# Kernel optimization log

Measured on AMD Instinct MI355X. Metric: run time of the kernel, lower is better.

The kernel has to match this reference:

```python
import jax, jax.numpy as jnp
import numpy as np

N_INIT = jnp.array([17.047, 14.099, 3.625], dtype=jnp.float32)
CA_INIT = jnp.array([16.967, 12.784, 4.338], dtype=jnp.float32)
C_INIT = jnp.array([15.685, 12.755, 5.133], dtype=jnp.float32)


def _unit(x):
    return x / (jnp.linalg.norm(x, axis=-1, keepdims=True) + 1e-8)


def _place_dihedral(a, b, c, bond_angle, bond_length, torsion):
    # a,b,c: [B,3]; bond_angle/bond_length/torsion: [B]
    ab = b - a
    bc = _unit(c - b)
    cr = jnp.cross(ab, bc)
    crn = jnp.linalg.norm(cr, axis=-1, keepdims=True)
    n_main = _unit(cr)
    # collinear fallback (per-element; almost never triggers for real angles)
    perp = jnp.zeros_like(bc).at[..., 0].set(1.0)
    ct = jnp.cross(bc, perp)
    ctn = jnp.linalg.norm(ct, axis=-1, keepdims=True)
    perp2 = jnp.where(ctn < 1e-6, jnp.zeros_like(bc).at[..., 1].set(1.0), perp)
    n_fb = _unit(jnp.cross(bc, perp2))
    n = jnp.where(crn < 1e-6, n_fb, n_main)
    nbc = jnp.cross(n, bc)
    m = jnp.stack([bc, nbc, n], axis=-1)  # [B,3,3]
    d_local = jnp.stack([
        -bond_length * jnp.cos(bond_angle),
        bond_length * jnp.cos(torsion) * jnp.sin(bond_angle),
        bond_length * jnp.sin(torsion) * jnp.sin(bond_angle),
    ], axis=-1)  # [B,3]
    d = jnp.einsum('bij,bj->bi', m, d_local)
    return d + c


def _nerf_build(phi, psi, omega, bond_lengths, bond_angles):
    B, L = phi.shape
    init = jnp.broadcast_to(jnp.stack([N_INIT, CA_INIT, C_INIT]), (B, 3, 3))
    # per-step params, leading axis = residue index i in [0, L-2]
    xs = (
        psi[:, :L - 1].T,                 # psi_i
        omega[:, :L - 1].T,               # omega_i
        phi[:, 1:].T,                     # phi_{i+1}
        bond_lengths[:, :L - 1, 2].T,     # C-N length
        bond_lengths[:, :L - 1, 0].T,     # N-CA length
        bond_lengths[:, :L - 1, 1].T,     # CA-C length
        bond_angles[:, :L - 1, 1].T,      # CA-C-N angle
        bond_angles[:, :L - 1, 2].T,      # C-N-CA angle
        bond_angles[:, :L - 1, 0].T,      # N-CA-C angle
    )

    def step(prev, x):
        psi_i, omega_i, phi_i, len_cn, len_nca, len_cac, ang_cacn, ang_cnca, ang_ncac = x
        a, b, c = prev[:, 0], prev[:, 1], prev[:, 2]
        n = _place_dihedral(a, b, c, ang_cacn, len_cn, psi_i)
        ca = _place_dihedral(b, c, n, ang_cnca, len_nca, omega_i)
        cc = _place_dihedral(c, n, ca, ang_ncac, len_cac, phi_i)
        new = jnp.stack([n, ca, cc], axis=1)  # [B,3,3]
        return new, new

    _, outs = jax.lax.scan(step, init, xs)  # [L-1,B,3,3]
    rest = outs.transpose(1, 0, 2, 3).reshape(B, 3 * (L - 1), 3)
    return jnp.concatenate([init, rest], axis=1)  # [B, 3L, 3]


def setup_inputs() -> dict:
    key = jax.random.key(0)
    k0, k1, k2, k3, k4 = jax.random.split(key, 5)
    B, L = 4096, 512
    phi = jax.random.normal(k0, (B, L), dtype=jnp.float32)
    psi = jax.random.normal(k1, (B, L), dtype=jnp.float32)
    omega = jax.random.normal(k2, (B, L), dtype=jnp.float32)
    # realistic positive bond lengths (~1.0-1.5 A) and bond angles (~1.5-2.3 rad)
    bond_lengths = 1.0 + 0.5 * jax.random.uniform(k3, (B, L, 3), dtype=jnp.float32)
    bond_angles = 1.5 + 0.8 * jax.random.uniform(k4, (B, L, 3), dtype=jnp.float32)
    return {"phi": phi, "psi": psi, "omega": omega,
            "bond_lengths": bond_lengths, "bond_angles": bond_angles}


def reference(phi, psi, omega, bond_lengths, bond_angles):
    return _nerf_build(phi, psi, omega, bond_lengths, bond_angles)
```

## Files before the change

kernel.cpp:

```cpp
#include <hip/hip_runtime.h>
#include <math.h>


#define LCH 512

struct Xf { float r[9]; float t[3]; };

__device__ __forceinline__ Xf xf_compose(const Xf& A, const Xf& B) {
  Xf C;
#pragma unroll
  for (int i = 0; i < 3; ++i) {
    float a0 = A.r[3*i+0], a1 = A.r[3*i+1], a2 = A.r[3*i+2];
    C.r[3*i+0] = a0*B.r[0] + a1*B.r[3] + a2*B.r[6];
    C.r[3*i+1] = a0*B.r[1] + a1*B.r[4] + a2*B.r[7];
    C.r[3*i+2] = a0*B.r[2] + a1*B.r[5] + a2*B.r[8];
    C.t[i]     = a0*B.t[0] + a1*B.t[1] + a2*B.t[2] + A.t[i];
  }
  return C;
}

__device__ __forceinline__ void xf_step(Xf& P, float theta, float len, float tau) {
  float st, ct, sx, cx;
  __sincosf(theta, &st, &ct);
  __sincosf(tau, &sx, &cx);
  float ux = -ct, uy = cx*st, uz = sx*st;
  float v0 = -st, v1 = -ct*cx, v2 = -ct*sx;
  float c00 = P.r[0]*ux + P.r[1]*uy + P.r[2]*uz;
  float c10 = P.r[3]*ux + P.r[4]*uy + P.r[5]*uz;
  float c20 = P.r[6]*ux + P.r[7]*uy + P.r[8]*uz;
  float c01 = P.r[0]*v0 + P.r[1]*v1 + P.r[2]*v2;
  float c11 = P.r[3]*v0 + P.r[4]*v1 + P.r[5]*v2;
  float c21 = P.r[6]*v0 + P.r[7]*v1 + P.r[8]*v2;
  float c02 = P.r[2]*cx - P.r[1]*sx;
  float c12 = P.r[5]*cx - P.r[4]*sx;
  float c22 = P.r[8]*cx - P.r[7]*sx;
  P.t[0] += len*c00; P.t[1] += len*c10; P.t[2] += len*c20;
  P.r[0]=c00; P.r[1]=c01; P.r[2]=c02;
  P.r[3]=c10; P.r[4]=c11; P.r[5]=c12;
  P.r[6]=c20; P.r[7]=c21; P.r[8]=c22;
}

__device__ __forceinline__ void xf_set_delta(Xf& P, float theta, float len, float tau) {
  float st, ct, sx, cx;
  __sincosf(theta, &st, &ct);
  __sincosf(tau, &sx, &cx);
  float ux = -ct, uy = cx*st, uz = sx*st;
  P.r[0]=ux; P.r[1]=-st;    P.r[2]=0.f;
  P.r[3]=uy; P.r[4]=-ct*cx; P.r[5]=-sx;
  P.r[6]=uz; P.r[7]=-ct*sx; P.r[8]=cx;
  P.t[0]=len*ux; P.t[1]=len*uy; P.t[2]=len*uz;
}

__device__ __forceinline__ void xf_identity(Xf& A) {
  A.r[0]=1.f; A.r[1]=0.f; A.r[2]=0.f;
  A.r[3]=0.f; A.r[4]=1.f; A.r[5]=0.f;
  A.r[6]=0.f; A.r[7]=0.f; A.r[8]=1.f;
  A.t[0]=0.f; A.t[1]=0.f; A.t[2]=0.f;
}

__device__ __forceinline__ Xf xf_shfl_up(const Xf& P, int d) {
  Xf O;
#pragma unroll
  for (int i = 0; i < 9; ++i) O.r[i] = __shfl_up(P.r[i], d, 64);
#pragma unroll
  for (int i = 0; i < 3; ++i) O.t[i] = __shfl_up(P.t[i], d, 64);
  return O;
}

__device__ __forceinline__ void xf_load_lds(const float* p, Xf& A) {
#pragma unroll
  for (int i = 0; i < 9; ++i) A.r[i] = p[i];
#pragma unroll
  for (int i = 0; i < 3; ++i) A.t[i] = p[9+i];
}

__global__ __launch_bounds__(256) void nerf_r6_kernel(
    const float* __restrict__ g_phi, const float* __restrict__ g_psi,
    const float* __restrict__ g_omg, const float* __restrict__ g_bl,
    const float* __restrict__ g_ba, float* __restrict__ g_out)
{
  __shared__ float s_tot[48];
  __shared__ float s_out[4608];

  const int t    = threadIdx.x;
  const int lane = t & 63;
  const int wave = t >> 6;
  const int chain = blockIdx.x;

  const float* phir = g_phi + (size_t)chain * LCH;
  const float* psir = g_psi + (size_t)chain * LCH;
  const float* omgr = g_omg + (size_t)chain * LCH;
  const float* blr  = g_bl  + (size_t)chain * LCH * 3;
  const float* bar  = g_ba  + (size_t)chain * LCH * 3;

  const int jm = (2*t - 1) > 0 ? (2*t - 1) : 0;
  const int jo = 2*t;

  float psiA = psir[jm], psiB = psir[jo];
  float omgA = omgr[jm], omgB = omgr[jo];
  float phiA = phir[jo], phiB = phir[jo + 1];
  float blA0 = blr[3*jm+0], blA1 = blr[3*jm+1], blA2 = blr[3*jm+2];
  float blB0 = blr[3*jo+0], blB1 = blr[3*jo+1], blB2 = blr[3*jo+2];
  float baA0 = bar[3*jm+0], baA1 = bar[3*jm+1], baA2 = bar[3*jm+2];
  float baB0 = bar[3*jo+0], baB1 = bar[3*jo+1], baB2 = bar[3*jo+2];

  Xf P;
  xf_set_delta(P, baA1, blA2, psiA);
  xf_step(P, baA2, blA0, omgA);
  xf_step(P, baA0, blA1, phiA);
  if (t == 0) xf_identity(P);
  xf_step(P, baB1, blB2, psiB);
  xf_step(P, baB2, blB0, omgB);
  xf_step(P, baB0, blB1, phiB);

#pragma unroll
  for (int d = 1; d < 64; d <<= 1) {
    Xf O = xf_shfl_up(P, d);
    if (lane >= d) P = xf_compose(O, P);
  }

  if (lane == 63) {
#pragma unroll
    for (int i = 0; i < 9; ++i) s_tot[12*wave + i] = P.r[i];
#pragma unroll
    for (int i = 0; i < 3; ++i) s_tot[12*wave + 9 + i] = P.t[i];
  }
  Xf E = xf_shfl_up(P, 1);
  __syncthreads();

  Xf A;
  {
    const float ax=17.047f, ay=14.099f, az=3.625f;
    const float bx_=16.967f, by_=12.784f, bz_=4.338f;
    const float cx_=15.685f, cy_=12.755f, cz_=5.133f;
    float abx=bx_-ax, aby=by_-ay, abz=bz_-az;
    float vx=cx_-bx_, vy=cy_-by_, vz=cz_-bz_;
    float vn = sqrtf(vx*vx+vy*vy+vz*vz) + 1e-8f;
    vx/=vn; vy/=vn; vz/=vn;
    float crx = aby*vz - abz*vy;
    float cry = abz*vx - abx*vz;
    float crz = abx*vy - aby*vx;
    float cn = sqrtf(crx*crx+cry*cry+crz*crz) + 1e-8f;
    float nx=crx/cn, ny=cry/cn, nz=crz/cn;
    float mx = ny*vz - nz*vy;
    float my = nz*vx - nx*vz;
    float mz = nx*vy - ny*vx;
    A.r[0]=vx; A.r[1]=mx; A.r[2]=nx;
    A.r[3]=vy; A.r[4]=my; A.r[5]=ny;
    A.r[6]=vz; A.r[7]=mz; A.r[8]=nz;
    A.t[0]=cx_; A.t[1]=cy_; A.t[2]=cz_;
  }
  if (wave >= 1) { Xf T; xf_load_lds(&s_tot[0],  T); A = xf_compose(A, T); }
  if (wave >= 2) { Xf T; xf_load_lds(&s_tot[12], T); A = xf_compose(A, T); }
  if (wave >= 3) { Xf T; xf_load_lds(&s_tot[24], T); A = xf_compose(A, T); }
  if (lane > 0) A = xf_compose(A, E);

  float* o = s_out + 18 * t;
  if (t == 0) {
    o[0]=17.047f; o[1]=14.099f; o[2]=3.625f;
    o[3]=16.967f; o[4]=12.784f; o[5]=4.338f;
    o[6]=15.685f; o[7]=12.755f; o[8]=5.133f;
  } else {
    xf_step(A, baA1, blA2, psiA);
    o[0]=A.t[0]; o[1]=A.t[1]; o[2]=A.t[2];
    xf_step(A, baA2, blA0, omgA);
    o[3]=A.t[0]; o[4]=A.t[1]; o[5]=A.t[2];
    xf_step(A, baA0, blA1, phiA);
    o[6]=A.t[0]; o[7]=A.t[1]; o[8]=A.t[2];
  }
  xf_step(A, baB1, blB2, psiB);
  o[9]=A.t[0];  o[10]=A.t[1]; o[11]=A.t[2];
  xf_step(A, baB2, blB0, omgB);
  o[12]=A.t[0]; o[13]=A.t[1]; o[14]=A.t[2];
  xf_step(A, baB0, blB1, phiB);
  o[15]=A.t[0]; o[16]=A.t[1]; o[17]=A.t[2];
  __syncthreads();

  float* orow = g_out + (size_t)chain * 4608;
#pragma unroll
  for (int q = 0; q < 9; ++q) {
    int g = 2*t + 512*q;
    float x = s_out[g];
    float y = s_out[g + 1];
    orow[g]     = x;
    orow[g + 1] = y;
  }
}

extern "C" void kernel_launch(void* const* d_in, const int* in_sizes, int n_in,
                              void* d_out, int out_size, void* d_ws, size_t ws_size,
                              hipStream_t stream) {
  const float* phi = (const float*)d_in[0];
  const float* psi = (const float*)d_in[1];
  const float* omg = (const float*)d_in[2];
  const float* bl  = (const float*)d_in[3];
  const float* ba  = (const float*)d_in[4];
  float* out = (float*)d_out;
  const int B = in_sizes[0] / LCH;
  hipLaunchKernelGGL(nerf_r6_kernel, dim3(B), dim3(256), 0, stream,
                     phi, psi, omg, bl, ba, out);
}
```

Before: 144.1 us.

## Map one chain per wavefront with 8 residues per lane and local-frame outputs

Each chain is now handled by a single 64-lane wavefront instead of a 256-thread block, so every lane processes 8 residues (24 atoms) in sequence. Lanes record local positions during their serial pass and apply the scanned prefix transform at the end, which removes the second stepping pass. This drops the cross-wave LDS reduction, both __syncthreads and the LDS output staging. Loads and stores become per-lane float4 vector accesses, at the cost of many more registers per thread (lower occupancy) and strided, less coalesced global access.

```diff
diff --git a/kernel.cpp b/kernel.cpp
--- a/kernel.cpp
+++ b/kernel.cpp
@@ -67,66 +67,102 @@
   return O;
 }
 
-__device__ __forceinline__ void xf_load_lds(const float* p, Xf& A) {
-#pragma unroll
-  for (int i = 0; i < 9; ++i) A.r[i] = p[i];
-#pragma unroll
-  for (int i = 0; i < 3; ++i) A.t[i] = p[9+i];
-}
-
-__global__ __launch_bounds__(256) void nerf_r6_kernel(
+__global__ __launch_bounds__(256) void nerf_r7_kernel(
     const float* __restrict__ g_phi, const float* __restrict__ g_psi,
     const float* __restrict__ g_omg, const float* __restrict__ g_bl,
-    const float* __restrict__ g_ba, float* __restrict__ g_out)
+    const float* __restrict__ g_ba, float* __restrict__ g_out, int nchain)
 {
-  __shared__ float s_tot[48];
-  __shared__ float s_out[4608];
-
-  const int t    = threadIdx.x;
-  const int lane = t & 63;
-  const int wave = t >> 6;
-  const int chain = blockIdx.x;
+  const int lane  = threadIdx.x & 63;
+  const int wave  = threadIdx.x >> 6;
+  const int chain = blockIdx.x * 4 + wave;
+  if (chain >= nchain) return;
 
   const float* phir = g_phi + (size_t)chain * LCH;
   const float* psir = g_psi + (size_t)chain * LCH;
   const float* omgr = g_omg + (size_t)chain * LCH;
-  const float* blr  = g_bl  + (size_t)chain * LCH * 3;
-  const float* bar  = g_ba  + (size_t)chain * LCH * 3;
-
-  const int jm = (2*t - 1) > 0 ? (2*t - 1) : 0;
-  const int jo = 2*t;
-
-  float psiA = psir[jm], psiB = psir[jo];
-  float omgA = omgr[jm], omgB = omgr[jo];
-  float phiA = phir[jo], phiB = phir[jo + 1];
-  float blA0 = blr[3*jm+0], blA1 = blr[3*jm+1], blA2 = blr[3*jm+2];
-  float blB0 = blr[3*jo+0], blB1 = blr[3*jo+1], blB2 = blr[3*jo+2];
-  float baA0 = bar[3*jm+0], baA1 = bar[3*jm+1], baA2 = bar[3*jm+2];
-  float baB0 = bar[3*jo+0], baB1 = bar[3*jo+1], baB2 = bar[3*jo+2];
+  const float* blr  = g_bl  + (size_t)chain * (LCH*3);
+  const float* bar  = g_ba  + (size_t)chain * (LCH*3);
+
+  const int j8  = 8 * lane;
+  const int b24 = 24 * lane;
+
+  float PS[8], OM[8], PH[8], BL[24], BA[24];
+  {
+    float  e0 = psir[j8 ? j8 - 1 : 0];
+    float4 v0 = *(const float4*)(psir + j8);
+    float2 v1 = *(const float2*)(psir + j8 + 4);
+    float  e7 = psir[j8 + 6];
+    PS[0]=e0; PS[1]=v0.x; PS[2]=v0.y; PS[3]=v0.z; PS[4]=v0.w; PS[5]=v1.x; PS[6]=v1.y; PS[7]=e7;
+  }
+  {
+    float  e0 = omgr[j8 ? j8 - 1 : 0];
+    float4 v0 = *(const float4*)(omgr + j8);
+    float2 v1 = *(const float2*)(omgr + j8 + 4);
+    float  e7 = omgr[j8 + 6];
+    OM[0]=e0; OM[1]=v0.x; OM[2]=v0.y; OM[3]=v0.z; OM[4]=v0.w; OM[5]=v1.x; OM[6]=v1.y; OM[7]=e7;
+  }
+  {
+    float4 v0 = *(const float4*)(phir + j8);
+    float4 v1 = *(const float4*)(phir + j8 + 4);
+    PH[0]=v0.x; PH[1]=v0.y; PH[2]=v0.z; PH[3]=v0.w;
+    PH[4]=v1.x; PH[5]=v1.y; PH[6]=v1.z; PH[7]=v1.w;
+  }
+  {
+    float  e0  = blr[b24 >= 3 ? b24 - 3 : 0];
+    float2 e12 = *(const float2*)(blr + (b24 >= 2 ? b24 - 2 : 0));
+    float4 w0 = *(const float4*)(blr + b24);
+    float4 w1 = *(const float4*)(blr + b24 + 4);
+    float4 w2 = *(const float4*)(blr + b24 + 8);
+    float4 w3 = *(const float4*)(blr + b24 + 12);
+    float4 w4 = *(const float4*)(blr + b24 + 16);
+    float  e23 = blr[b24 + 20];
+    BL[0]=e0;   BL[1]=e12.x; BL[2]=e12.y;
+    BL[3]=w0.x; BL[4]=w0.y;  BL[5]=w0.z;  BL[6]=w0.w;
+    BL[7]=w1.x; BL[8]=w1.y;  BL[9]=w1.z;  BL[10]=w1.w;
+    BL[11]=w2.x; BL[12]=w2.y; BL[13]=w2.z; BL[14]=w2.w;
+    BL[15]=w3.x; BL[16]=w3.y; BL[17]=w3.z; BL[18]=w3.w;
+    BL[19]=w4.x; BL[20]=w4.y; BL[21]=w4.z; BL[22]=w4.w;
+    BL[23]=e23;
+  }
+  {
+    float  e0  = bar[b24 >= 3 ? b24 - 3 : 0];
+    float2 e12 = *(const float2*)(bar + (b24 >= 2 ? b24 - 2 : 0));
+    float4 w0 = *(const float4*)(bar + b24);
+    float4 w1 = *(const float4*)(bar + b24 + 4);
+    float4 w2 = *(const float4*)(bar + b24 + 8);
+    float4 w3 = *(const float4*)(bar + b24 + 12);
+    float4 w4 = *(const float4*)(bar + b24 + 16);
+    float  e23 = bar[b24 + 20];
+    BA[0]=e0;   BA[1]=e12.x; BA[2]=e12.y;
+    BA[3]=w0.x; BA[4]=w0.y;  BA[5]=w0.z;  BA[6]=w0.w;
+    BA[7]=w1.x; BA[8]=w1.y;  BA[9]=w1.z;  BA[10]=w1.w;
+    BA[11]=w2.x; BA[12]=w2.y; BA[13]=w2.z; BA[14]=w2.w;
+    BA[15]=w3.x; BA[16]=w3.y; BA[17]=w3.z; BA[18]=w3.w;
+    BA[19]=w4.x; BA[20]=w4.y; BA[21]=w4.z; BA[22]=w4.w;
+    BA[23]=e23;
+  }
 
   Xf P;
-  xf_set_delta(P, baA1, blA2, psiA);
-  xf_step(P, baA2, blA0, omgA);
-  xf_step(P, baA0, blA1, phiA);
-  if (t == 0) xf_identity(P);
-  xf_step(P, baB1, blB2, psiB);
-  xf_step(P, baB2, blB0, omgB);
-  xf_step(P, baB0, blB1, phiB);
+  float sx[24], sy[24], sz[24];
+#pragma unroll
+  for (int k = 0; k < 24; ++k) {
+    const int m = k / 3, a = k - 3*m;
+    float th, ln, ta;
+    if (a == 0)      { th = BA[3*m+1]; ln = BL[3*m+2]; ta = PS[m]; }
+    else if (a == 1) { th = BA[3*m+2]; ln = BL[3*m+0]; ta = OM[m]; }
+    else             { th = BA[3*m+0]; ln = BL[3*m+1]; ta = PH[m]; }
+    if (k == 0) xf_set_delta(P, th, ln, ta);
+    else        xf_step(P, th, ln, ta);
+    sx[k] = P.t[0]; sy[k] = P.t[1]; sz[k] = P.t[2];
+    if (k == 2 && lane == 0) xf_identity(P);
+  }
 
 #pragma unroll
   for (int d = 1; d < 64; d <<= 1) {
     Xf O = xf_shfl_up(P, d);
     if (lane >= d) P = xf_compose(O, P);
   }
-
-  if (lane == 63) {
-#pragma unroll
-    for (int i = 0; i < 9; ++i) s_tot[12*wave + i] = P.r[i];
-#pragma unroll
-    for (int i = 0; i < 3; ++i) s_tot[12*wave + 9 + i] = P.t[i];
-  }
   Xf E = xf_shfl_up(P, 1);
-  __syncthreads();
 
   Xf A;
   {
@@ -150,40 +186,27 @@
     A.r[6]=vz; A.r[7]=mz; A.r[8]=nz;
     A.t[0]=cx_; A.t[1]=cy_; A.t[2]=cz_;
   }
-  if (wave >= 1) { Xf T; xf_load_lds(&s_tot[0],  T); A = xf_compose(A, T); }
-  if (wave >= 2) { Xf T; xf_load_lds(&s_tot[12], T); A = xf_compose(A, T); }
-  if (wave >= 3) { Xf T; xf_load_lds(&s_tot[24], T); A = xf_compose(A, T); }
   if (lane > 0) A = xf_compose(A, E);
 
-  float* o = s_out + 18 * t;
-  if (t == 0) {
-    o[0]=17.047f; o[1]=14.099f; o[2]=3.625f;
-    o[3]=16.967f; o[4]=12.784f; o[5]=4.338f;
-    o[6]=15.685f; o[7]=12.755f; o[8]=5.133f;
-  } else {
-    xf_step(A, baA1, blA2, psiA);
-    o[0]=A.t[0]; o[1]=A.t[1]; o[2]=A.t[2];
-    xf_step(A, baA2, blA0, omgA);
-    o[3]=A.t[0]; o[4]=A.t[1]; o[5]=A.t[2];
-    xf_step(A, baA0, blA1, phiA);
-    o[6]=A.t[0]; o[7]=A.t[1]; o[8]=A.t[2];
-  }
-  xf_step(A, baB1, blB2, psiB);
-  o[9]=A.t[0];  o[10]=A.t[1]; o[11]=A.t[2];
-  xf_step(A, baB2, blB0, omgB);
-  o[12]=A.t[0]; o[13]=A.t[1]; o[14]=A.t[2];
-  xf_step(A, baB0, blB1, phiB);
-  o[15]=A.t[0]; o[16]=A.t[1]; o[17]=A.t[2];
-  __syncthreads();
-
-  float* orow = g_out + (size_t)chain * 4608;
-#pragma unroll
-  for (int q = 0; q < 9; ++q) {
-    int g = 2*t + 512*q;
-    float x = s_out[g];
-    float y = s_out[g + 1];
-    orow[g]     = x;
-    orow[g + 1] = y;
+  float out[72];
+#pragma unroll
+  for (int k = 0; k < 24; ++k) {
+    out[3*k+0] = A.r[0]*sx[k] + A.r[1]*sy[k] + A.r[2]*sz[k] + A.t[0];
+    out[3*k+1] = A.r[3]*sx[k] + A.r[4]*sy[k] + A.r[5]*sz[k] + A.t[1];
+    out[3*k+2] = A.r[6]*sx[k] + A.r[7]*sy[k] + A.r[8]*sz[k] + A.t[2];
+  }
+  if (lane == 0) {
+    out[0]=17.047f; out[1]=14.099f; out[2]=3.625f;
+    out[3]=16.967f; out[4]=12.784f; out[5]=4.338f;
+    out[6]=15.685f; out[7]=12.755f; out[8]=5.133f;
+  }
+
+  float* orow = g_out + (size_t)chain * 4608 + 72 * lane;
+#pragma unroll
+  for (int q = 0; q < 18; ++q) {
+    float4 v;
+    v.x = out[4*q+0]; v.y = out[4*q+1]; v.z = out[4*q+2]; v.w = out[4*q+3];
+    *(float4*)(orow + 4*q) = v;
   }
 }
 
@@ -197,6 +220,7 @@
   const float* ba  = (const float*)d_in[4];
   float* out = (float*)d_out;
   const int B = in_sizes[0] / LCH;
-  hipLaunchKernelGGL(nerf_r6_kernel, dim3(B), dim3(256), 0, stream,
-                     phi, psi, omg, bl, ba, out);
-}
+  const int blocks = (B + 3) / 4;
+  hipLaunchKernelGGL(nerf_r7_kernel, dim3(blocks), dim3(256), 0, stream,
+                     phi, psi, omg, bl, ba, out, B);
+}
```

Measured after the change: 160.1 us. 1.11x slower.
